# Performance work log

Hardware: AMD Instinct MI355X
Metric: run time of the kernel (lower is better)

The kernel has to match this reference:

```python
import jax, jax.numpy as jnp
import numpy as np

BETA = 1.0  # commitment loss weight (beta=1.0 in VQKD.__init__)

def l2norm(x, eps=1e-12):
    return x / jnp.maximum(jnp.linalg.norm(x, axis=-1, keepdims=True), eps)

def setup_inputs() -> dict:
    key = jax.random.key(0)
    k0, k1, k2, k3 = jax.random.split(key, 4)
    B, N, D_ENC, D_CODE, K = 8, 4096, 768, 32, 8192
    std = 0.02  # trunc_normal_(std=0.02) init of task layers
    return {
        "features": jax.random.normal(k0, (B, N, D_ENC), jnp.float32),
        "enc_w1": jax.random.normal(k1, (D_ENC, D_ENC), jnp.float32) * std,
        "enc_b1": jnp.zeros((D_ENC,), jnp.float32),
        "enc_w2": jax.random.normal(k2, (D_ENC, D_CODE), jnp.float32) * std,
        "enc_b2": jnp.zeros((D_CODE,), jnp.float32),
        "codebook": jax.random.normal(k3, (K, D_CODE), jnp.float32),
    }

def reference(features, enc_w1, enc_b1, enc_w2, enc_b2, codebook):
    # encode_task_layer: Linear -> Tanh -> Linear (run in fp32, as in the autocast-disabled block)
    z = jnp.tanh(features @ enc_w1 + enc_b1) @ enc_w2 + enc_b2          # [B, N, C]
    # NormEMAVectorQuantizer: l2-normalize tokens and (EMA-normalized) codebook
    z = l2norm(z)
    emb = l2norm(codebook)                                              # [K, C]
    # squared euclidean distances  ||z||^2 - 2 z.e + ||e||^2  -> [B, N, K]
    d = (jnp.sum(z * z, axis=-1, keepdims=True)
         - 2.0 * jnp.einsum('bnc,kc->bnk', z, emb)
         + jnp.sum(emb * emb, axis=-1))
    idx = jnp.argmin(d, axis=-1)                                        # [B, N] int32
    z_q_raw = emb[idx]                                                  # gather [B, N, C]
    loss = BETA * jnp.mean((jax.lax.stop_gradient(z_q_raw) - z) ** 2)   # commitment loss
    z_q = z + jax.lax.stop_gradient(z_q_raw - z)                        # straight-through
    return z_q, loss, idx
```

## Files before the change

### kernel.cpp

```cpp
#include <hip/hip_runtime.h>
#include <hip/hip_bf16.h>
#include <cstdint>
#include <cstddef>


namespace {
constexpr int TOKENS = 8 * 4096;
constexpr int DENC   = 768;
constexpr int DC     = 32;
constexpr int KC     = 8192;
constexpr int BM = 128, BN = 128, BK = 32;
constexpr int NSTEP = DENC / BK;
constexpr int NT    = DENC / BN;
constexpr int BUFSZ = 32768;
constexpr float WSCALE = 1024.0f;
constexpr float HSCALE = 512.0f;
constexpr float SSCALE = 512.0f;
constexpr int SCH = 256;
}

typedef _Float16 f16x8 __attribute__((ext_vector_type(8)));
typedef float    f32x4 __attribute__((ext_vector_type(4)));

__device__ inline void split2(float v, _Float16& h, _Float16& l) {
  h = (_Float16)v;
  l = (_Float16)(v - (float)h);
}

__device__ inline void gload_lds16(const void* g, void* l) {
  __builtin_amdgcn_global_load_lds(
      (const __attribute__((address_space(1))) void*)g,
      (__attribute__((address_space(3))) void*)l, 16, 0, 0);
}

__global__ void ksplitW(const float* __restrict__ W1,
                        _Float16* __restrict__ Wh, _Float16* __restrict__ Wl) {
  int n = blockIdx.y;
  int k = blockIdx.x * 256 + threadIdx.x;
  float w = W1[(size_t)k * DENC + n] * WSCALE;
  _Float16 h, l; split2(w, h, l);
  Wh[(size_t)n * DENC + k] = h;
  Wl[(size_t)n * DENC + k] = l;
}

__global__ void ksplitW2(const float* __restrict__ W2,
                         _Float16* __restrict__ W2h, _Float16* __restrict__ W2l) {
  int i = blockIdx.x * 256 + threadIdx.x;
  int k = i >> 5, c = i & 31;
  float w = W2[(size_t)k * DC + c] * WSCALE;
  _Float16 h, l; split2(w, h, l);
  W2h[(size_t)c * DENC + k] = h;
  W2l[(size_t)c * DENC + k] = l;
}

__global__ void knorm_codes(const float* __restrict__ cb,
                            float* __restrict__ embn, float* __restrict__ se2,
                            _Float16* __restrict__ Eh, _Float16* __restrict__ El) {
  int t = blockIdx.x * blockDim.x + threadIdx.x;
  int k = t >> 5, c = t & 31;
  float v = cb[(size_t)k * DC + c];
  float ss = v * v;
  #pragma unroll
  for (int m = 16; m >= 1; m >>= 1) ss += __shfl_xor(ss, m, 32);
  float nrm = fmaxf(sqrtf(ss), 1e-12f);
  float vn = v / nrm;
  embn[(size_t)k * DC + c] = vn;
  _Float16 h, l; split2(vn * SSCALE, h, l);
  Eh[(size_t)k * DC + c] = h;
  El[(size_t)k * DC + c] = l;
  float s2 = vn * vn;
  #pragma unroll
  for (int m = 16; m >= 1; m >>= 1) s2 += __shfl_xor(s2, m, 32);
  if (c == 0) se2[k] = s2 * (SSCALE * SSCALE);
}

__global__ __launch_bounds__(256, 2)
void kfused(const float* __restrict__ X,
            const _Float16* __restrict__ Wh, const _Float16* __restrict__ Wl,
            const float* __restrict__ bias1,
            const _Float16* __restrict__ W2h, const _Float16* __restrict__ W2l,
            float* __restrict__ zpart) {
  __shared__ __align__(16) char smem[2 * BUFSZ];
  float (*Hs)[68] = (float(*)[68])smem;

  const int bid = blockIdx.x;
  const int xcd = bid & 7;
  const int w   = bid >> 3;
  const int n_t = w % 6;
  const int m_t = xcd * 32 + w / 6;
  const int m0 = m_t * BM, n0 = n_t * BN;

  const int t    = threadIdx.x;
  const int lane = t & 63;
  const int wv   = t >> 6;
  const int wm   = wv >> 1, wn = wv & 1;
  const int lrow = lane & 15;
  const int lgrp = lane >> 4;

  const int ae = (lane & 1) ^ ((lane >> 3) & 1);
  const float* xsrcA = X + (size_t)(m0 + wv * 32 + (lane >> 1)) * DENC + ae * 4;
  const _Float16* bsrc[2] = {
    Wh + (size_t)(n0 + (wv & 1) * 64 + lane) * DENC,
    Wl + (size_t)(n0 + (wv & 1) * 64 + lane) * DENC };
  const int bko_half = wv >> 1;

  f32x4 acc[4][4];
  #pragma unroll
  for (int i = 0; i < 4; ++i)
    #pragma unroll
    for (int j = 0; j < 4; ++j) acc[i][j] = (f32x4)0.0f;

  auto stage = [&](char* buf, int s) {
    const int k0 = s * BK;
    #pragma unroll
    for (int r = 0; r < 4; ++r)
      gload_lds16(xsrcA + k0 + r * 8, buf + r * 4096 + wv * 1024);
    char* bbuf = buf + 16384;
    #pragma unroll
    for (int r = 0; r < 4; ++r) {
      const int pl = r >> 1;
      const int ko = (r & 1) * 2 + bko_half;
      gload_lds16(bsrc[pl] + k0 + ko * 8, bbuf + r * 4096 + wv * 1024);
    }
  };

  stage(smem, 0);
  __syncthreads();

  for (int s = 0; s < NSTEP; ++s) {
    char* bufc = smem + (size_t)(s & 1) * BUFSZ;
    if (s + 1 < NSTEP) stage(smem + (size_t)((s + 1) & 1) * BUFSZ, s + 1);

    f16x8 fah[4], fal[4];
    #pragma unroll
    for (int mf = 0; mf < 4; ++mf) {
      const int row = wm * 64 + mf * 16 + lrow;
      const int b   = (row >> 2) & 1;
      const char* base = bufc + lgrp * 4096 + row * 32;
      float4 u = *(const float4*)(base + ((0 ^ b) << 4));
      float4 v = *(const float4*)(base + ((1 ^ b) << 4));
      float va[8] = {u.x, u.y, u.z, u.w, v.x, v.y, v.z, v.w};
      f16x8 hh, ll;
      #pragma unroll
      for (int e = 0; e < 8; ++e) { _Float16 h, l; split2(va[e], h, l); hh[e] = h; ll[e] = l; }
      fah[mf] = hh; fal[mf] = ll;
    }

    const _Float16* Bsm = (const _Float16*)(bufc + 16384);
    #pragma unroll
    for (int nf = 0; nf < 4; ++nf) {
      const int col = wn * 64 + nf * 16 + lrow;
      f16x8 nbh = *(const f16x8*)&Bsm[((0 * 4 + lgrp) * BN + col) * 8];
      f16x8 nbl = *(const f16x8*)&Bsm[((1 * 4 + lgrp) * BN + col) * 8];
      #pragma unroll
      for (int mf = 0; mf < 4; ++mf) {
        acc[mf][nf] = __builtin_amdgcn_mfma_f32_16x16x32_f16(fah[mf], nbh, acc[mf][nf], 0, 0, 0);
        acc[mf][nf] = __builtin_amdgcn_mfma_f32_16x16x32_f16(fah[mf], nbl, acc[mf][nf], 0, 0, 0);
        acc[mf][nf] = __builtin_amdgcn_mfma_f32_16x16x32_f16(fal[mf], nbh, acc[mf][nf], 0, 0, 0);
      }
    }

    __syncthreads();
  }

  {
    float bv[4];
    #pragma unroll
    for (int nf = 0; nf < 4; ++nf) bv[nf] = bias1[n0 + wn * 64 + nf * 16 + lrow];
    #pragma unroll
    for (int mf = 0; mf < 4; ++mf)
      #pragma unroll
      for (int nf = 0; nf < 4; ++nf)
        #pragma unroll
        for (int r = 0; r < 4; ++r)
          acc[mf][nf][r] = tanhf(acc[mf][nf][r] * (1.0f / WSCALE) + bv[nf]);
  }

  f32x4 zacc[2][2];
  #pragma unroll
  for (int i = 0; i < 2; ++i)
    #pragma unroll
    for (int j = 0; j < 2; ++j) zacc[i][j] = (f32x4)0.0f;

  #pragma unroll
  for (int h = 0; h < 2; ++h) {
    __syncthreads();
    if (wn == h) {
      #pragma unroll
      for (int mf = 0; mf < 4; ++mf)
        #pragma unroll
        for (int nf = 0; nf < 4; ++nf)
          #pragma unroll
          for (int r = 0; r < 4; ++r)
            Hs[wm * 64 + mf * 16 + lgrp * 4 + r][nf * 16 + lrow] = acc[mf][nf][r];
    }
    __syncthreads();
    #pragma unroll
    for (int ks = 0; ks < 2; ++ks) {
      const int koct = ks * 4 + lgrp;
      f16x8 bfh[2], bfl[2];
      #pragma unroll
      for (int nf = 0; nf < 2; ++nf) {
        const int c = nf * 16 + lrow;
        const size_t kg = (size_t)c * DENC + n0 + h * 64 + koct * 8;
        bfh[nf] = *(const f16x8*)&W2h[kg];
        bfl[nf] = *(const f16x8*)&W2l[kg];
      }
      #pragma unroll
      for (int mf = 0; mf < 2; ++mf) {
        const float* hp = &Hs[wv * 32 + mf * 16 + lrow][koct * 8];
        float4 u = *(const float4*)hp, v = *(const float4*)(hp + 4);
        float va[8] = {u.x, u.y, u.z, u.w, v.x, v.y, v.z, v.w};
        f16x8 hh, ll;
        #pragma unroll
        for (int e = 0; e < 8; ++e) { _Float16 hx, lx; split2(va[e] * HSCALE, hx, lx); hh[e] = hx; ll[e] = lx; }
        #pragma unroll
        for (int nf = 0; nf < 2; ++nf) {
          zacc[mf][nf] = __builtin_amdgcn_mfma_f32_16x16x32_f16(hh, bfh[nf], zacc[mf][nf], 0, 0, 0);
          zacc[mf][nf] = __builtin_amdgcn_mfma_f32_16x16x32_f16(hh, bfl[nf], zacc[mf][nf], 0, 0, 0);
          zacc[mf][nf] = __builtin_amdgcn_mfma_f32_16x16x32_f16(ll, bfh[nf], zacc[mf][nf], 0, 0, 0);
        }
      }
    }
  }

  float* zp = zpart + (size_t)n_t * TOKENS * DC;
  #pragma unroll
  for (int mf = 0; mf < 2; ++mf)
    #pragma unroll
    for (int r = 0; r < 4; ++r) {
      const int row = m0 + wv * 32 + mf * 16 + lgrp * 4 + r;
      #pragma unroll
      for (int nf = 0; nf < 2; ++nf)
        zp[(size_t)row * DC + nf * 16 + lrow] = zacc[mf][nf][r];
    }
}

__global__ void kreduce(const float* __restrict__ zpart, const float* __restrict__ b2,
                        float* __restrict__ zn) {
  int t = blockIdx.x * blockDim.x + threadIdx.x;
  int c = t & 31;
  float s = 0.0f;
  #pragma unroll
  for (int nt = 0; nt < NT; ++nt) s += zpart[(size_t)nt * TOKENS * DC + t];
  float z = s * (1.0f / (HSCALE * WSCALE)) + b2[c];
  float ss = z * z;
  #pragma unroll
  for (int m = 16; m >= 1; m >>= 1) ss += __shfl_xor(ss, m, 32);
  float nrm = fmaxf(sqrtf(ss), 1e-12f);
  zn[t] = z / nrm;
}

__device__ inline unsigned long long packkey(float d, int idx) {
  unsigned int u = __float_as_uint(d);
  u = (u & 0x80000000u) ? ~u : (u | 0x80000000u);
  return ((unsigned long long)u << 32) | (unsigned int)idx;
}

__global__ __launch_bounds__(256, 4)
void ksearch(const float* __restrict__ zn, const _Float16* __restrict__ Eh,
             const _Float16* __restrict__ El, const float* __restrict__ se2,
             unsigned long long* __restrict__ keys) {
  __shared__ __align__(16) _Float16 Bh[4][SCH][8], Bl[4][SCH][8];
  __shared__ float ce2[SCH];
  const int t = threadIdx.x, lane = t & 63, wv = t >> 6;
  const int tb  = blockIdx.x * 256 + wv * 64;
  const int cb0 = blockIdx.y * 1024;
  const int lr = lane & 15, ko = lane >> 4;

  f16x8 azh[4], azl[4];
  #pragma unroll
  for (int m = 0; m < 4; ++m) {
    const float* zp = zn + (size_t)(tb + m * 16 + lr) * DC + ko * 8;
    float4 u = *(const float4*)zp, v = *(const float4*)(zp + 4);
    float vals[8] = {u.x, u.y, u.z, u.w, v.x, v.y, v.z, v.w};
    f16x8 hh, ll;
    #pragma unroll
    for (int e = 0; e < 8; ++e) {
      _Float16 h, l; split2(vals[e] * SSCALE, h, l);
      hh[e] = h; ll[e] = l;
    }
    azh[m] = hh; azl[m] = ll;
  }

  float best[4][4]; int bi[4][4];
  #pragma unroll
  for (int m = 0; m < 4; ++m)
    #pragma unroll
    for (int r = 0; r < 4; ++r) { best[m][r] = 3.4e38f; bi[m][r] = 0; }

  f16x8 pb[8]; float pe2;

  for (int ch = 0; ch < 4; ++ch) {
    const int cb = cb0 + ch * SCH;
    #pragma unroll
    for (int it = 0; it < 8; ++it) {
      const _Float16* src = (it < 4) ? Eh : El;
      pb[it] = *(const f16x8*)&src[(size_t)(cb + t) * DC + (it & 3) * 8];
    }
    pe2 = se2[cb + t];
    __syncthreads();
    #pragma unroll
    for (int it = 0; it < 8; ++it) {
      _Float16 (*B)[SCH][8] = (it < 4) ? Bh : Bl;
      *(f16x8*)&B[it & 3][t][0] = pb[it];
    }
    ce2[t] = pe2;
    __syncthreads();

    #pragma unroll 4
    for (int f = 0; f < SCH / 16; ++f) {
      f16x8 bh = *(const f16x8*)&Bh[ko][f * 16 + lr][0];
      f16x8 bl = *(const f16x8*)&Bl[ko][f * 16 + lr][0];
      float e2v = ce2[f * 16 + lr];
      int  code = cb + f * 16 + lr;
      #pragma unroll
      for (int m = 0; m < 4; ++m) {
        f32x4 a = (f32x4)0.0f;
        a = __builtin_amdgcn_mfma_f32_16x16x32_f16(azh[m], bh, a, 0, 0, 0);
        a = __builtin_amdgcn_mfma_f32_16x16x32_f16(azh[m], bl, a, 0, 0, 0);
        a = __builtin_amdgcn_mfma_f32_16x16x32_f16(azl[m], bh, a, 0, 0, 0);
        #pragma unroll
        for (int r = 0; r < 4; ++r) {
          float d = fmaf(-2.0f, a[r], e2v);
          bool c = d < best[m][r];
          best[m][r] = c ? d : best[m][r];
          bi[m][r]   = c ? code : bi[m][r];
        }
      }
    }
  }

  #pragma unroll
  for (int m = 0; m < 4; ++m)
    #pragma unroll
    for (int r = 0; r < 4; ++r) {
      float bd = best[m][r]; int ix = bi[m][r];
      #pragma unroll
      for (int s = 1; s < 16; s <<= 1) {
        float od = __shfl_xor(bd, s);
        int   oi = __shfl_xor(ix, s);
        if (od < bd || (od == bd && oi < ix)) { bd = od; ix = oi; }
      }
      if ((lane & 15) == 0) {
        int token = tb + m * 16 + (lane >> 4) * 4 + r;
        atomicMin(&keys[token], packkey(bd, ix));
      }
    }
}

__global__ __launch_bounds__(1024)
void kfinal(const unsigned long long* __restrict__ keys,
            const float* __restrict__ zn, const float* __restrict__ embn,
            float* __restrict__ zq, float* __restrict__ loss,
            float* __restrict__ oidx) {
  __shared__ float red[32];
  int t = blockIdx.x * blockDim.x + threadIdx.x;
  int tok = t >> 5, c = t & 31;
  unsigned long long key = keys[tok];
  int idx = (int)(unsigned int)(key & 0xFFFFFFFFull);
  float q = embn[(size_t)idx * DC + c];
  float z = zn[t];
  zq[t] = z + (q - z);
  float d = q - z;
  float ss = d * d;
  #pragma unroll
  for (int m = 16; m >= 1; m >>= 1) ss += __shfl_xor(ss, m, 32);
  if (c == 0) {
    red[threadIdx.x >> 5] = ss;
    oidx[tok] = (float)idx;
  }
  __syncthreads();
  if (threadIdx.x < 32) {
    float v = red[threadIdx.x];
    #pragma unroll
    for (int m = 16; m >= 1; m >>= 1) v += __shfl_xor(v, m, 32);
    if (threadIdx.x == 0)
      atomicAdd(loss, v * (1.0f / (float)(TOKENS * DC)));
  }
}

extern "C" void kernel_launch(void* const* d_in, const int* in_sizes, int n_in,
                              void* d_out, int out_size, void* d_ws, size_t ws_size,
                              hipStream_t stream) {
  const float* X   = (const float*)d_in[0];
  const float* W1  = (const float*)d_in[1];
  const float* B1  = (const float*)d_in[2];
  const float* W2  = (const float*)d_in[3];
  const float* B2  = (const float*)d_in[4];
  const float* CB  = (const float*)d_in[5];

  float* out  = (float*)d_out;
  float* zq   = out;
  float* loss = out + (size_t)TOKENS * DC;
  float* oidx = loss + 1;

  char* ws = (char*)d_ws;
  size_t off = 0;
  float* zpart = (float*)(ws + off); off += (size_t)NT * TOKENS * DC * 4;
  float* zn   = (float*)(ws + off); off += (size_t)TOKENS * DC * 4;
  float* embn = (float*)(ws + off); off += (size_t)KC * DC * 4;
  float* se2  = (float*)(ws + off); off += (size_t)KC * 4;
  _Float16* Eh = (_Float16*)(ws + off); off += (size_t)KC * DC * 2;
  _Float16* El = (_Float16*)(ws + off); off += (size_t)KC * DC * 2;
  unsigned long long* keys = (unsigned long long*)(ws + off);
  off += (size_t)TOKENS * 8;
  _Float16* W2h = (_Float16*)(ws + off); off += (size_t)DC * DENC * 2;
  _Float16* W2l = (_Float16*)(ws + off); off += (size_t)DC * DENC * 2;
  _Float16* W1h = (_Float16*)zn;
  _Float16* W1l = W1h + (size_t)DENC * DENC;

  hipMemsetAsync(loss, 0, sizeof(float), stream);
  hipMemsetAsync(keys, 0xFF, (size_t)TOKENS * 8, stream);

  ksplitW<<<dim3(DENC / 256, DENC), 256, 0, stream>>>(W1, W1h, W1l);
  ksplitW2<<<(DENC * DC) / 256, 256, 0, stream>>>(W2, W2h, W2l);
  knorm_codes<<<(KC * DC) / 256, 256, 0, stream>>>(CB, embn, se2, Eh, El);
  kfused<<<(TOKENS / BM) * (DENC / BN), 256, 0, stream>>>(X, W1h, W1l, B1, W2h, W2l, zpart);
  kreduce<<<TOKENS * DC / 256, 256, 0, stream>>>(zpart, B2, zn);
  ksearch<<<dim3(TOKENS / 256, KC / 1024), 256, 0, stream>>>(zn, Eh, El, se2, keys);
  kfinal<<<TOKENS * DC / 1024, 1024, 0, stream>>>(keys, zn, embn, zq, loss, oidx);
}
```

Measured before the change: 271.1 us.

## Prefetch two K-steps ahead with explicit vmcnt waits in fused GEMM

The first GEMM's mainloop is restructured so that tiles for steps s and s+1 are in flight together. Each iteration waits with s_waitcnt vmcnt(8) and a raw s_barrier, computes on one buffer, then issues the load for step s+2 into the buffer it just freed. A and B tiles now sit in separate 16 KB regions, and the XOR swizzle on the A tile layout is removed. The aim is to hide more global load latency behind the MFMA work. Dropping the swizzle may bring back LDS bank conflicts on the A-fragment reads.

After: 271.6 us. About the same (+0.2%).

```diff
diff --git a/kernel.cpp b/kernel.cpp
--- a/kernel.cpp
+++ b/kernel.cpp
@@ -12,7 +12,6 @@
 constexpr int BM = 128, BN = 128, BK = 32;
 constexpr int NSTEP = DENC / BK;
 constexpr int NT    = DENC / BN;
-constexpr int BUFSZ = 32768;
 constexpr float WSCALE = 1024.0f;
 constexpr float HSCALE = 512.0f;
 constexpr float SSCALE = 512.0f;
@@ -80,7 +79,7 @@
             const float* __restrict__ bias1,
             const _Float16* __restrict__ W2h, const _Float16* __restrict__ W2l,
             float* __restrict__ zpart) {
-  __shared__ __align__(16) char smem[2 * BUFSZ];
+  __shared__ __align__(16) char smem[65536];
   float (*Hs)[68] = (float(*)[68])smem;
 
   const int bid = blockIdx.x;
@@ -97,8 +96,7 @@
   const int lrow = lane & 15;
   const int lgrp = lane >> 4;
 
-  const int ae = (lane & 1) ^ ((lane >> 3) & 1);
-  const float* xsrcA = X + (size_t)(m0 + wv * 32 + (lane >> 1)) * DENC + ae * 4;
+  const float* xsrcA = X + (size_t)(m0 + wv * 32 + (lane >> 1)) * DENC + (lane & 1) * 4;
   const _Float16* bsrc[2] = {
     Wh + (size_t)(n0 + (wv & 1) * 64 + lane) * DENC,
     Wl + (size_t)(n0 + (wv & 1) * 64 + lane) * DENC };
@@ -110,43 +108,36 @@
     #pragma unroll
     for (int j = 0; j < 4; ++j) acc[i][j] = (f32x4)0.0f;
 
-  auto stage = [&](char* buf, int s) {
+  auto stage = [&](int s, int buf) {
     const int k0 = s * BK;
+    char* ab = smem + buf * 16384;
+    char* bb = smem + 32768 + buf * 16384;
     #pragma unroll
     for (int r = 0; r < 4; ++r)
-      gload_lds16(xsrcA + k0 + r * 8, buf + r * 4096 + wv * 1024);
-    char* bbuf = buf + 16384;
+      gload_lds16(xsrcA + k0 + r * 8, ab + r * 4096 + wv * 1024);
     #pragma unroll
     for (int r = 0; r < 4; ++r) {
-      const int pl = r >> 1;
-      const int ko = (r & 1) * 2 + bko_half;
-      gload_lds16(bsrc[pl] + k0 + ko * 8, bbuf + r * 4096 + wv * 1024);
+      const int pl = r >> 1, ko = (r & 1) * 2 + bko_half;
+      gload_lds16(bsrc[pl] + k0 + ko * 8, bb + r * 4096 + wv * 1024);
     }
   };
 
-  stage(smem, 0);
-  __syncthreads();
-
-  for (int s = 0; s < NSTEP; ++s) {
-    char* bufc = smem + (size_t)(s & 1) * BUFSZ;
-    if (s + 1 < NSTEP) stage(smem + (size_t)((s + 1) & 1) * BUFSZ, s + 1);
-
+  auto compute = [&](int buf) {
+    const char* abase = smem + buf * 16384;
+    const _Float16* Bsm = (const _Float16*)(smem + 32768 + buf * 16384);
     f16x8 fah[4], fal[4];
     #pragma unroll
     for (int mf = 0; mf < 4; ++mf) {
       const int row = wm * 64 + mf * 16 + lrow;
-      const int b   = (row >> 2) & 1;
-      const char* base = bufc + lgrp * 4096 + row * 32;
-      float4 u = *(const float4*)(base + ((0 ^ b) << 4));
-      float4 v = *(const float4*)(base + ((1 ^ b) << 4));
+      const char* p = abase + lgrp * 4096 + row * 32;
+      float4 u = *(const float4*)p;
+      float4 v = *(const float4*)(p + 16);
       float va[8] = {u.x, u.y, u.z, u.w, v.x, v.y, v.z, v.w};
       f16x8 hh, ll;
       #pragma unroll
       for (int e = 0; e < 8; ++e) { _Float16 h, l; split2(va[e], h, l); hh[e] = h; ll[e] = l; }
       fah[mf] = hh; fal[mf] = ll;
     }
-
-    const _Float16* Bsm = (const _Float16*)(bufc + 16384);
     #pragma unroll
     for (int nf = 0; nf < 4; ++nf) {
       const int col = wn * 64 + nf * 16 + lrow;
@@ -159,9 +150,27 @@
         acc[mf][nf] = __builtin_amdgcn_mfma_f32_16x16x32_f16(fal[mf], nbh, acc[mf][nf], 0, 0, 0);
       }
     }
-
-    __syncthreads();
-  }
+  };
+
+  stage(0, 0);
+  stage(1, 1);
+  #pragma unroll 1
+  for (int s = 0; s < NSTEP - 1; ++s) {
+    asm volatile("s_waitcnt vmcnt(8)" ::: "memory");
+    __builtin_amdgcn_sched_barrier(0);
+    __builtin_amdgcn_s_barrier();
+    __builtin_amdgcn_sched_barrier(0);
+    compute(s & 1);
+    __builtin_amdgcn_sched_barrier(0);
+    __builtin_amdgcn_s_barrier();
+    __builtin_amdgcn_sched_barrier(0);
+    if (s + 2 < NSTEP) stage(s + 2, s & 1);
+  }
+  asm volatile("s_waitcnt vmcnt(0)" ::: "memory");
+  __builtin_amdgcn_sched_barrier(0);
+  __builtin_amdgcn_s_barrier();
+  __builtin_amdgcn_sched_barrier(0);
+  compute((NSTEP - 1) & 1);
 
   {
     float bv[4];
```
